# Performance work log

Measured on AMD Instinct MI355X. Metric: run time of the kernel, lower is better.

Reference implementation:

```python
import jax, jax.numpy as jnp
import numpy as np

B, S, D = 4, 2048, 1024   # batch, seq_len, input feature dim
H, E = 16, 64             # head_num, att_embedding_size; H*E = model dim


def setup_inputs() -> dict:
    key = jax.random.key(0)
    ks = jax.random.split(key, 9)
    std = 1.0 / np.sqrt(D)
    M = H * E
    return {
        "x": jax.random.normal(ks[0], (B, S, D), dtype=jnp.float32),
        "Wq": jax.random.normal(ks[1], (D, M), dtype=jnp.float32) * std,
        "bq": jnp.zeros((M,), dtype=jnp.float32),
        "Wk": jax.random.normal(ks[2], (D, M), dtype=jnp.float32) * std,
        "bk": jnp.zeros((M,), dtype=jnp.float32),
        "Wv": jax.random.normal(ks[3], (D, M), dtype=jnp.float32) * std,
        "bv": jnp.zeros((M,), dtype=jnp.float32),
        "Wr": jax.random.normal(ks[4], (D, M), dtype=jnp.float32) * std,
        "br": jnp.zeros((M,), dtype=jnp.float32),
    }


def reference(x, Wq, bq, Wk, bk, Wv, bv, Wr, br):
    # QKV dense layers with ReLU activation (as in the original Keras code)
    qw = jax.nn.relu(x @ Wq + bq)                      # [B,S,H*E]
    kw = jax.nn.relu(x @ Wk + bk)
    vw = jax.nn.relu(x @ Wv + bv)
    # split heads: [B,S,H,E] -> [B,H,S,E]
    qw = qw.reshape(B, S, H, E).transpose(0, 2, 1, 3)
    kw = kw.reshape(B, S, H, E).transpose(0, 2, 1, 3)
    vw = vw.reshape(B, S, H, E).transpose(0, 2, 1, 3)
    # unscaled attention (original has no 1/sqrt(d) scaling)
    a = jnp.einsum("bhqe,bhke->bhqk", qw, kw)          # [B,H,S,S]
    a = jax.nn.softmax(a, axis=-1)
    o = jnp.einsum("bhqk,bhke->bhqe", a, vw)           # [B,H,S,E]
    o = o.transpose(0, 2, 1, 3).reshape(B, S, H * E)
    # residual dense (no activation)
    o = o + (x @ Wr + br)
    return o
```

## Files before the change

kernel.cpp:

```cpp
#include <hip/hip_runtime.h>


typedef __bf16 bf16x8 __attribute__((ext_vector_type(8)));
typedef float  f32x4  __attribute__((ext_vector_type(4)));
typedef short  short8 __attribute__((ext_vector_type(8)));
typedef short  short4v __attribute__((ext_vector_type(4)));
typedef float  float4v __attribute__((ext_vector_type(4)));
typedef int    int4v  __attribute__((ext_vector_type(4)));
typedef unsigned uint2v __attribute__((ext_vector_type(2)));

#define LOG2E 1.44269504088896f

__device__ __forceinline__ unsigned short f2bf(float f) {
  unsigned u = __builtin_bit_cast(unsigned, f);
  u += 0x7fffu + ((u >> 16) & 1u);
  return (unsigned short)(u >> 16);
}

__device__ __forceinline__ unsigned pack2(float lo, float hi) {
  __bf16 a = (__bf16)lo, b = (__bf16)hi;
  unsigned short ua = __builtin_bit_cast(unsigned short, a);
  unsigned short ub = __builtin_bit_cast(unsigned short, b);
  return (unsigned)ua | ((unsigned)ub << 16);
}

__global__ __launch_bounds__(256) void k_cvt_x(const float* __restrict__ x,
                                               short* __restrict__ Xb) {
  const size_t i = ((size_t)blockIdx.x * 256 + threadIdx.x) * 4;
  float4v f = *(const float4v*)(x + i);
  short4v o;
  o[0] = (short)f2bf(f[0]); o[1] = (short)f2bf(f[1]);
  o[2] = (short)f2bf(f[2]); o[3] = (short)f2bf(f[3]);
  *(short4v*)(Xb + i) = o;
}

__global__ __launch_bounds__(256) void k_cvt_w(const float* __restrict__ Wq,
                                               const float* __restrict__ Wk,
                                               const float* __restrict__ Wv,
                                               const float* __restrict__ Wr,
                                               short* __restrict__ Wc) {
  const int bid = blockIdx.x;
  const int w = bid >> 8;
  const int t = bid & 255;
  const int tr = t >> 4, tc = t & 15;
  const float* Ws = (w == 0) ? Wq : (w == 1) ? Wk : (w == 2) ? Wv : Wr;
  __shared__ float T[64][65];
  const int tx = threadIdx.x & 63, ty = threadIdx.x >> 6;
#pragma unroll
  for (int i = 0; i < 16; ++i)
    T[i * 4 + ty][tx] = Ws[(size_t)(tr * 64 + i * 4 + ty) * 1024 + tc * 64 + tx];
  __syncthreads();
#pragma unroll
  for (int i = 0; i < 16; ++i) {
    const int n = tc * 64 + i * 4 + ty;
    Wc[((size_t)w * 1024 + n) * 1024 + tr * 64 + tx] = (short)f2bf(T[tx][i * 4 + ty]);
  }
}

__global__ __launch_bounds__(512, 2) void k_gemm(const short* __restrict__ Xb,
                                                 const short* __restrict__ Wc,
                                                 const float* __restrict__ bq,
                                                 const float* __restrict__ bk2,
                                                 const float* __restrict__ bv,
                                                 const float* __restrict__ br,
                                                 short* __restrict__ Qb,
                                                 short* __restrict__ Kb,
                                                 short* __restrict__ Vt,
                                                 float* __restrict__ Out) {
  __shared__ __align__(16) short smem[65536];
  char* const sb = (char*)smem;
  const int tid = threadIdx.x, wid = tid >> 6, lane = tid & 63;
  const int lr = lane & 15, hi = lane >> 4;
  const int bm = blockIdx.x & 31, bn = blockIdx.x >> 5;
  const int m0 = bm * 256, n0 = bn * 256;
  const int wm = wid >> 2, wn = wid & 3;

  f32x4 acc[8][4] = {};

  const int sl_ = (tid & 7) ^ ((tid >> 3) & 7);
  const int rA0 = ((tid >> 3) << 1) + (sl_ >> 2);
  const short* sa0 = Xb + (size_t)(m0 + rA0) * 1024 + (sl_ & 3) * 8;
  const short* sa1 = Xb + (size_t)(m0 + 128 + rA0) * 1024 + (sl_ & 3) * 8;
  const short* sg0 = Wc + (size_t)(n0 + rA0) * 1024 + (sl_ & 3) * 8;
  const short* sg1 = Wc + (size_t)(n0 + 128 + rA0) * 1024 + (sl_ & 3) * 8;

  const int xr = (((lane & 1) * 4 + hi) ^ ((lr >> 1) & 7)) * 16;
  const int amb = wm * 8192 + (lr >> 1) * 128 + xr;
  const int bnb = 65536 + wn * 4096 + (lr >> 1) * 128 + xr;

#define GLL(SRC, LDSOFF)                                                                   \
  __builtin_amdgcn_global_load_lds((const __attribute__((address_space(1))) void*)(SRC),   \
      (__attribute__((address_space(3))) void*)(sb + (LDSOFF)), 16, 0, 0)

#define STAGE(SLOT)                                                                        \
  do {                                                                                     \
    GLL(sa0, (SLOT) * 16384 + wid * 1024);                                                 \
    GLL(sa1, (SLOT) * 16384 + 8192 + wid * 1024);                                          \
    GLL(sg0, 65536 + (SLOT) * 16384 + wid * 1024);                                         \
    GLL(sg1, 65536 + (SLOT) * 16384 + 8192 + wid * 1024);                                  \
    sa0 += 32; sa1 += 32; sg0 += 32; sg1 += 32;                                            \
  } while (0)

#define PHASE(J, VM, STG)                                                                  \
  do {                                                                                     \
    asm volatile("s_waitcnt vmcnt(" #VM ")" ::: "memory");                                 \
    __builtin_amdgcn_sched_barrier(0);                                                     \
    __builtin_amdgcn_s_barrier();                                                          \
    __builtin_amdgcn_sched_barrier(0);                                                     \
    if (STG) STAGE(((J) + 3) & 3);                                                         \
    bf16x8 am[8], bnr[4];                                                                  \
    _Pragma("unroll")                                                                      \
    for (int mf = 0; mf < 8; ++mf)                                                         \
      am[mf] = *(const bf16x8*)(sb + (((J) & 3) * 16384 + amb + mf * 1024));               \
    _Pragma("unroll")                                                                      \
    for (int nf = 0; nf < 4; ++nf)                                                         \
      bnr[nf] = *(const bf16x8*)(sb + (((J) & 3) * 16384 + bnb + nf * 1024));              \
    asm volatile("s_waitcnt lgkmcnt(0)" ::: "memory");                                     \
    __builtin_amdgcn_sched_barrier(0);                                                     \
    __builtin_amdgcn_s_setprio(1);                                                         \
    _Pragma("unroll")                                                                      \
    for (int mf = 0; mf < 8; ++mf)                                                         \
      _Pragma("unroll")                                                                    \
      for (int nf = 0; nf < 4; ++nf)                                                       \
        acc[mf][nf] = __builtin_amdgcn_mfma_f32_16x16x32_bf16(am[mf], bnr[nf],             \
                                                              acc[mf][nf], 0, 0, 0);      \
    __builtin_amdgcn_s_setprio(0);                                                         \
    __builtin_amdgcn_sched_barrier(0);                                                     \
  } while (0)

  STAGE(0);
  STAGE(1);
  STAGE(2);

  for (int it = 0; it < 7; ++it) {
    PHASE(0, 8, 1);
    PHASE(1, 8, 1);
    PHASE(2, 8, 1);
    PHASE(3, 8, 1);
  }
  PHASE(0, 8, 1);
  PHASE(1, 8, 0);
  PHASE(2, 4, 0);
  PHASE(3, 0, 0);
#undef PHASE
#undef STAGE
#undef GLL

#pragma unroll
  for (int mf = 0; mf < 8; ++mf) {
    const int mbase = m0 + wm * 128 + mf * 16 + hi * 4;
    const int bb2 = mbase >> 11, sbase = mbase & 2047;
#pragma unroll
    for (int nf = 0; nf < 4; ++nf) {
      const int n = n0 + wn * 64 + nf * 16 + lr;
      const float* bp = (n < 2048) ? (n < 1024 ? bq : bk2) : (n < 3072 ? bv : br);
      const float bias = bp[n & 1023];
      float v[4];
#pragma unroll
      for (int r = 0; r < 4; ++r) v[r] = acc[mf][nf][r] + bias;

      if (n < 2048) {
        const int nn = n & 1023, h = nn >> 6, e = nn & 63;
        short* dst = (n < 1024) ? Qb : Kb;
#pragma unroll
        for (int r = 0; r < 4; ++r)
          dst[(((size_t)bb2 * 16 + h) * 2048 + sbase + r) * 64 + e] = (short)f2bf(fmaxf(v[r], 0.f));
      } else if (n < 3072) {
        const int nn = n & 1023, h = nn >> 6, e = nn & 63;
        const int kq = sbase & 31;
        const int Sp = (sbase & ~31) + ((kq >> 2) & 3) * 8 + (kq >> 4) * 4;
        uint2v pv;
        pv[0] = pack2(fmaxf(v[0], 0.f), fmaxf(v[1], 0.f));
        pv[1] = pack2(fmaxf(v[2], 0.f), fmaxf(v[3], 0.f));
        *(uint2v*)&Vt[(((size_t)bb2 * 16 + h) * 64 + e) * 2048 + Sp] = pv;
      } else {
#pragma unroll
        for (int r = 0; r < 4; ++r)
          Out[(size_t)(mbase + r) * 1024 + (n - 3072)] = v[r];
      }
    }
  }
}

__global__ __launch_bounds__(256, 2) void k_attn(const short* __restrict__ Qb,
                                                 const short* __restrict__ Kb,
                                                 const short* __restrict__ Vt,
                                                 float* __restrict__ Out) {
  __shared__ __align__(16) short smem[16384];
  char* const sb = (char*)smem;
  const int tid = threadIdx.x, wid = tid >> 6, lane = tid & 63;
  const int lr = lane & 15, hi = lane >> 4;
  const int bid = ((blockIdx.x & 7) << 6) | (blockIdx.x >> 3);
  const int bh = bid >> 3;
  const int q0 = (bid & 7) * 256;
  const size_t hb = (size_t)bh * (2048 * 64);

  bf16x8 aq[4][2];
#pragma unroll
  for (int g = 0; g < 4; ++g) {
    const short* qp = Qb + hb + (size_t)(q0 + wid * 64 + g * 16 + lr) * 64 + hi * 8;
    aq[g][0] = *(const bf16x8*)qp;
    aq[g][1] = *(const bf16x8*)(qp + 32);
  }

  f32x4 o[4][4] = {};
  float l_run[4] = {0.f, 0.f, 0.f, 0.f};

  const int swz = ((lane & 7) ^ (lane >> 3)) * 8;
  const int rlo = lane >> 3;
  const int wr0 = wid * 16;
  const short* kp0 = Kb + hb + (size_t)(wr0 + rlo) * 64 + swz;
  const short* kp1 = kp0 + 8 * 64;
  const short* vp0 = Vt + hb + (size_t)(wr0 + rlo) * 2048 + swz;
  const short* vp1 = vp0 + 8 * 2048;

  const int vb0 = (lr * 64 + ((hi ^ (lr & 7)) << 3)) * 2;
  const int vb1 = vb0 ^ 64;

#define GLL(SRC, LDSOFF)                                                                   \
  __builtin_amdgcn_global_load_lds((const __attribute__((address_space(1))) void*)(SRC),   \
      (__attribute__((address_space(3))) void*)(sb + (LDSOFF)), 16, 0, 0)

  GLL(kp0, wr0 * 128);
  GLL(kp1, wr0 * 128 + 1024);
  GLL(vp0, 16384 + wr0 * 128);
  GLL(vp1, 16384 + wr0 * 128 + 1024);
  kp0 += 4096; kp1 += 4096; vp0 += 64; vp1 += 64;

  for (int kt = 0; kt < 32; ++kt) {
    const int buf = kt & 1;
    if (kt < 31) {
      const int d = (buf ^ 1) * 8192 + wr0 * 128;
      GLL(kp0, d);
      GLL(kp1, d + 1024);
      GLL(vp0, 16384 + d);
      GLL(vp1, 16384 + d + 1024);
      kp0 += 4096; kp1 += 4096; vp0 += 64; vp1 += 64;
      asm volatile("s_waitcnt vmcnt(4)" ::: "memory");
    } else {
      asm volatile("s_waitcnt vmcnt(0)" ::: "memory");
    }
    __builtin_amdgcn_sched_barrier(0);
    __builtin_amdgcn_s_barrier();
    __builtin_amdgcn_sched_barrier(0);

    f32x4 s[4][4];
    __builtin_amdgcn_s_setprio(1);
#pragma unroll
    for (int kc = 0; kc < 4; ++kc) {
      const bf16x8 kf0 = *(const bf16x8*)(sb + (vb0 + buf * 8192 + kc * 2048));
      const bf16x8 kf1 = *(const bf16x8*)(sb + (vb1 + buf * 8192 + kc * 2048));
#pragma unroll
      for (int g = 0; g < 4; ++g) {
        f32x4 t = __builtin_amdgcn_mfma_f32_16x16x32_bf16(kf0, aq[g][0], (f32x4){0.f, 0.f, 0.f, 0.f}, 0, 0, 0);
        s[g][kc] = __builtin_amdgcn_mfma_f32_16x16x32_bf16(kf1, aq[g][1], t, 0, 0, 0);
      }
    }
    __builtin_amdgcn_s_setprio(0);

    int4v pw[4][2];
#pragma unroll
    for (int g = 0; g < 4; ++g) {
      float sum = 0.f;
#pragma unroll
      for (int kc = 0; kc < 4; ++kc) {
        const float p0 = __builtin_amdgcn_exp2f(s[g][kc][0] * LOG2E);
        const float p1 = __builtin_amdgcn_exp2f(s[g][kc][1] * LOG2E);
        const float p2 = __builtin_amdgcn_exp2f(s[g][kc][2] * LOG2E);
        const float p3 = __builtin_amdgcn_exp2f(s[g][kc][3] * LOG2E);
        sum += (p0 + p1) + (p2 + p3);
        pw[g][kc >> 1][(kc & 1) * 2] = (int)pack2(p0, p1);
        pw[g][kc >> 1][(kc & 1) * 2 + 1] = (int)pack2(p2, p3);
      }
      l_run[g] += sum;
    }

    __builtin_amdgcn_s_setprio(1);
#pragma unroll
    for (int kk = 0; kk < 2; ++kk) {
      const int cb = (kk ? vb1 : vb0) + 16384 + buf * 8192;
#pragma unroll
      for (int et = 0; et < 4; ++et) {
        const bf16x8 vf = *(const bf16x8*)(sb + (cb + et * 2048));
#pragma unroll
        for (int g = 0; g < 4; ++g)
          o[g][et] = __builtin_amdgcn_mfma_f32_16x16x32_bf16(
              vf, __builtin_bit_cast(bf16x8, pw[g][kk]), o[g][et], 0, 0, 0);
      }
    }
    __builtin_amdgcn_s_setprio(0);

    asm volatile("s_waitcnt lgkmcnt(0)" ::: "memory");
    __builtin_amdgcn_sched_barrier(0);
    __builtin_amdgcn_s_barrier();
    __builtin_amdgcn_sched_barrier(0);
  }

  float* Ep = (float*)smem + wid * 1088;
  const int b = bh >> 4, h = bh & 15;
  const int qr = lane >> 2, cc = lane & 3;
#pragma unroll
  for (int g = 0; g < 4; ++g) {
    float lt = l_run[g];
    lt += __shfl_xor(lt, 16);
    lt += __shfl_xor(lt, 32);
    const float inv = 1.0f / lt;
#pragma unroll
    for (int et = 0; et < 4; ++et) {
      f32x4 v = o[g][et] * inv;
      *(float4v*)&Ep[lr * 68 + et * 16 + hi * 4] = v;
    }
    asm volatile("s_waitcnt lgkmcnt(0)" ::: "memory");
    const size_t gb = ((size_t)b * 2048 + q0 + wid * 64 + g * 16 + qr) * 1024 + h * 64 + cc * 4;
#pragma unroll
    for (int i = 0; i < 4; ++i) {
      float4v v = *(const float4v*)&Ep[qr * 68 + cc * 4 + i * 16];
      float4v u = *(const float4v*)&Out[gb + i * 16];
      u += v;
      *(float4v*)&Out[gb + i * 16] = u;
    }
    asm volatile("s_waitcnt lgkmcnt(0)" ::: "memory");
  }
#undef GLL
}

extern "C" void kernel_launch(void* const* d_in, const int* in_sizes, int n_in,
                              void* d_out, int out_size, void* d_ws, size_t ws_size,
                              hipStream_t stream) {
  const float* x  = (const float*)d_in[0];
  const float* Wq = (const float*)d_in[1];
  const float* bq = (const float*)d_in[2];
  const float* Wk = (const float*)d_in[3];
  const float* bk = (const float*)d_in[4];
  const float* Wv = (const float*)d_in[5];
  const float* bv = (const float*)d_in[6];
  const float* Wr = (const float*)d_in[7];
  const float* br = (const float*)d_in[8];
  float* Out = (float*)d_out;

  char* ws = (char*)d_ws;
  short* Xb = (short*)(ws);
  short* Wc = (short*)(ws + (size_t)16 * 1024 * 1024);
  short* Qb = (short*)(ws + (size_t)24 * 1024 * 1024);
  short* Kb = (short*)(ws + (size_t)40 * 1024 * 1024);
  short* Vt = (short*)(ws + (size_t)56 * 1024 * 1024);

  k_cvt_x<<<8192, 256, 0, stream>>>(x, Xb);
  k_cvt_w<<<1024, 256, 0, stream>>>(Wq, Wk, Wv, Wr, Wc);
  k_gemm<<<512, 512, 0, stream>>>(Xb, Wc, bq, bk, bv, br, Qb, Kb, Vt, Out);
  k_attn<<<512, 256, 0, stream>>>(Qb, Kb, Vt, Out);
}
```

Before: 172.8 us.

## Software-pipeline attention: 4-stage LDS ring, overlap QK of next tile with PV

Restructures the attention main loop into a four-slot LDS ring buffer with three tiles in flight. Each iteration issues the QK MFMAs for the next tile together with the PV MFMAs for the current tile, then runs the softmax exp after the barrier, so MFMA work and exp/VALU work can interleave across waves. It also folds LOG2E into Q when Q is written out in the projection kernel, removing a multiply per score. LDS use doubles to 64KB per block, which may reduce occupancy below the two blocks per CU requested by the launch bounds.

```diff
diff --git a/kernel.cpp b/kernel.cpp
--- a/kernel.cpp
+++ b/kernel.cpp
@@ -162,9 +162,11 @@
       if (n < 2048) {
         const int nn = n & 1023, h = nn >> 6, e = nn & 63;
         short* dst = (n < 1024) ? Qb : Kb;
+        const float scale = (n < 1024) ? LOG2E : 1.0f;
 #pragma unroll
         for (int r = 0; r < 4; ++r)
-          dst[(((size_t)bb2 * 16 + h) * 2048 + sbase + r) * 64 + e] = (short)f2bf(fmaxf(v[r], 0.f));
+          dst[(((size_t)bb2 * 16 + h) * 2048 + sbase + r) * 64 + e] =
+              (short)f2bf(fmaxf(v[r], 0.f) * scale);
       } else if (n < 3072) {
         const int nn = n & 1023, h = nn >> 6, e = nn & 63;
         const int kq = sbase & 31;
@@ -186,7 +188,7 @@
                                                  const short* __restrict__ Kb,
                                                  const short* __restrict__ Vt,
                                                  float* __restrict__ Out) {
-  __shared__ __align__(16) short smem[16384];
+  __shared__ __align__(16) short smem[32768];
   char* const sb = (char*)smem;
   const int tid = threadIdx.x, wid = tid >> 6, lane = tid & 63;
   const int lr = lane & 15, hi = lane >> 4;
@@ -205,6 +207,8 @@
 
   f32x4 o[4][4] = {};
   float l_run[4] = {0.f, 0.f, 0.f, 0.f};
+  f32x4 s[4][4];
+  int4v pw[4][2];
 
   const int swz = ((lane & 7) ^ (lane >> 3)) * 8;
   const int rlo = lane >> 3;
@@ -221,80 +225,110 @@
   __builtin_amdgcn_global_load_lds((const __attribute__((address_space(1))) void*)(SRC),   \
       (__attribute__((address_space(3))) void*)(sb + (LDSOFF)), 16, 0, 0)
 
-  GLL(kp0, wr0 * 128);
-  GLL(kp1, wr0 * 128 + 1024);
-  GLL(vp0, 16384 + wr0 * 128);
-  GLL(vp1, 16384 + wr0 * 128 + 1024);
-  kp0 += 4096; kp1 += 4096; vp0 += 64; vp1 += 64;
-
-  for (int kt = 0; kt < 32; ++kt) {
-    const int buf = kt & 1;
-    if (kt < 31) {
-      const int d = (buf ^ 1) * 8192 + wr0 * 128;
-      GLL(kp0, d);
-      GLL(kp1, d + 1024);
-      GLL(vp0, 16384 + d);
-      GLL(vp1, 16384 + d + 1024);
-      kp0 += 4096; kp1 += 4096; vp0 += 64; vp1 += 64;
-      asm volatile("s_waitcnt vmcnt(4)" ::: "memory");
-    } else {
-      asm volatile("s_waitcnt vmcnt(0)" ::: "memory");
-    }
-    __builtin_amdgcn_sched_barrier(0);
-    __builtin_amdgcn_s_barrier();
-    __builtin_amdgcn_sched_barrier(0);
-
-    f32x4 s[4][4];
-    __builtin_amdgcn_s_setprio(1);
-#pragma unroll
-    for (int kc = 0; kc < 4; ++kc) {
-      const bf16x8 kf0 = *(const bf16x8*)(sb + (vb0 + buf * 8192 + kc * 2048));
-      const bf16x8 kf1 = *(const bf16x8*)(sb + (vb1 + buf * 8192 + kc * 2048));
-#pragma unroll
-      for (int g = 0; g < 4; ++g) {
-        f32x4 t = __builtin_amdgcn_mfma_f32_16x16x32_bf16(kf0, aq[g][0], (f32x4){0.f, 0.f, 0.f, 0.f}, 0, 0, 0);
-        s[g][kc] = __builtin_amdgcn_mfma_f32_16x16x32_bf16(kf1, aq[g][1], t, 0, 0, 0);
-      }
-    }
-    __builtin_amdgcn_s_setprio(0);
-
-    int4v pw[4][2];
-#pragma unroll
-    for (int g = 0; g < 4; ++g) {
-      float sum = 0.f;
-#pragma unroll
-      for (int kc = 0; kc < 4; ++kc) {
-        const float p0 = __builtin_amdgcn_exp2f(s[g][kc][0] * LOG2E);
-        const float p1 = __builtin_amdgcn_exp2f(s[g][kc][1] * LOG2E);
-        const float p2 = __builtin_amdgcn_exp2f(s[g][kc][2] * LOG2E);
-        const float p3 = __builtin_amdgcn_exp2f(s[g][kc][3] * LOG2E);
-        sum += (p0 + p1) + (p2 + p3);
-        pw[g][kc >> 1][(kc & 1) * 2] = (int)pack2(p0, p1);
-        pw[g][kc >> 1][(kc & 1) * 2 + 1] = (int)pack2(p2, p3);
-      }
-      l_run[g] += sum;
-    }
-
-    __builtin_amdgcn_s_setprio(1);
-#pragma unroll
-    for (int kk = 0; kk < 2; ++kk) {
-      const int cb = (kk ? vb1 : vb0) + 16384 + buf * 8192;
-#pragma unroll
-      for (int et = 0; et < 4; ++et) {
-        const bf16x8 vf = *(const bf16x8*)(sb + (cb + et * 2048));
-#pragma unroll
-        for (int g = 0; g < 4; ++g)
-          o[g][et] = __builtin_amdgcn_mfma_f32_16x16x32_bf16(
-              vf, __builtin_bit_cast(bf16x8, pw[g][kk]), o[g][et], 0, 0, 0);
-      }
-    }
-    __builtin_amdgcn_s_setprio(0);
-
-    asm volatile("s_waitcnt lgkmcnt(0)" ::: "memory");
-    __builtin_amdgcn_sched_barrier(0);
-    __builtin_amdgcn_s_barrier();
-    __builtin_amdgcn_sched_barrier(0);
-  }
+#define STAGE(SLOT)                                                                        \
+  do {                                                                                     \
+    GLL(kp0, (SLOT) * 8192 + wr0 * 128);                                                   \
+    GLL(kp1, (SLOT) * 8192 + wr0 * 128 + 1024);                                            \
+    GLL(vp0, 32768 + (SLOT) * 8192 + wr0 * 128);                                           \
+    GLL(vp1, 32768 + (SLOT) * 8192 + wr0 * 128 + 1024);                                    \
+    kp0 += 4096; kp1 += 4096; vp0 += 64; vp1 += 64;                                        \
+  } while (0)
+
+#define QK(KS)                                                                             \
+  do {                                                                                     \
+    _Pragma("unroll")                                                                      \
+    for (int kc = 0; kc < 4; ++kc) {                                                       \
+      const bf16x8 kf0 = *(const bf16x8*)(sb + ((KS) * 8192 + vb0 + kc * 2048));           \
+      const bf16x8 kf1 = *(const bf16x8*)(sb + ((KS) * 8192 + vb1 + kc * 2048));           \
+      _Pragma("unroll")                                                                    \
+      for (int g = 0; g < 4; ++g) {                                                        \
+        f32x4 t = __builtin_amdgcn_mfma_f32_16x16x32_bf16(kf0, aq[g][0],                   \
+                                                          (f32x4){0.f, 0.f, 0.f, 0.f},    \
+                                                          0, 0, 0);                        \
+        s[g][kc] = __builtin_amdgcn_mfma_f32_16x16x32_bf16(kf1, aq[g][1], t, 0, 0, 0);     \
+      }                                                                                    \
+    }                                                                                      \
+  } while (0)
+
+#define PV(VS)                                                                             \
+  do {                                                                                     \
+    _Pragma("unroll")                                                                      \
+    for (int kk = 0; kk < 2; ++kk) {                                                       \
+      const int cb = (kk ? vb1 : vb0) + 32768 + (VS) * 8192;                               \
+      _Pragma("unroll")                                                                    \
+      for (int et = 0; et < 4; ++et) {                                                     \
+        const bf16x8 vf = *(const bf16x8*)(sb + (cb + et * 2048));                         \
+        _Pragma("unroll")                                                                  \
+        for (int g = 0; g < 4; ++g)                                                        \
+          o[g][et] = __builtin_amdgcn_mfma_f32_16x16x32_bf16(                              \
+              vf, __builtin_bit_cast(bf16x8, pw[g][kk]), o[g][et], 0, 0, 0);               \
+      }                                                                                    \
+    }                                                                                      \
+  } while (0)
+
+#define SM()                                                                               \
+  do {                                                                                     \
+    _Pragma("unroll")                                                                      \
+    for (int g = 0; g < 4; ++g) {                                                          \
+      float sum = 0.f;                                                                     \
+      _Pragma("unroll")                                                                    \
+      for (int kc = 0; kc < 4; ++kc) {                                                     \
+        const float p0 = __builtin_amdgcn_exp2f(s[g][kc][0]);                              \
+        const float p1 = __builtin_amdgcn_exp2f(s[g][kc][1]);                              \
+        const float p2 = __builtin_amdgcn_exp2f(s[g][kc][2]);                              \
+        const float p3 = __builtin_amdgcn_exp2f(s[g][kc][3]);                              \
+        sum += (p0 + p1) + (p2 + p3);                                                      \
+        pw[g][kc >> 1][(kc & 1) * 2] = (int)pack2(p0, p1);                                 \
+        pw[g][kc >> 1][(kc & 1) * 2 + 1] = (int)pack2(p2, p3);                             \
+      }                                                                                    \
+      l_run[g] += sum;                                                                     \
+    }                                                                                      \
+  } while (0)
+
+#define ITER(J, VM, STG)                                                                   \
+  do {                                                                                     \
+    if (STG) STAGE(((J) + 3) & 3);                                                         \
+    asm volatile("s_waitcnt vmcnt(" #VM ")" ::: "memory");                                 \
+    __builtin_amdgcn_sched_barrier(0);                                                     \
+    __builtin_amdgcn_s_barrier();                                                          \
+    __builtin_amdgcn_sched_barrier(0);                                                     \
+    __builtin_amdgcn_s_setprio(1);                                                         \
+    QK(((J) + 1) & 3);                                                                     \
+    PV((J) & 3);                                                                           \
+    __builtin_amdgcn_s_setprio(0);                                                         \
+    asm volatile("s_waitcnt lgkmcnt(0)" ::: "memory");                                     \
+    __builtin_amdgcn_sched_barrier(0);                                                     \
+    __builtin_amdgcn_s_barrier();                                                          \
+    __builtin_amdgcn_sched_barrier(0);                                                     \
+    SM();                                                                                  \
+  } while (0)
+
+  STAGE(0);
+  STAGE(1);
+  STAGE(2);
+  asm volatile("s_waitcnt vmcnt(8)" ::: "memory");
+  __builtin_amdgcn_sched_barrier(0);
+  __builtin_amdgcn_s_barrier();
+  __builtin_amdgcn_sched_barrier(0);
+  QK(0);
+  SM();
+
+  for (int it = 0; it < 7; ++it) {
+    ITER(0, 8, 1);
+    ITER(1, 8, 1);
+    ITER(2, 8, 1);
+    ITER(3, 8, 1);
+  }
+  ITER(0, 8, 1);
+  ITER(1, 4, 0);
+  ITER(2, 0, 0);
+  PV(3);
+#undef ITER
+#undef SM
+#undef PV
+#undef QK
+#undef STAGE
+#undef GLL
 
   float* Ep = (float*)smem + wid * 1088;
   const int b = bh >> 4, h = bh & 15;
@@ -321,7 +355,6 @@
     }
     asm volatile("s_waitcnt lgkmcnt(0)" ::: "memory");
   }
-#undef GLL
 }
 
 extern "C" void kernel_launch(void* const* d_in, const int* in_sizes, int n_in,
```

Result: slower. 440.8 us (+155.1%).

## Halve attention query tile per block and fold log2e scale into Q

Applied to the files above, without the earlier changes.

The attention kernel now gives each block 128 queries instead of 256, so each warp holds 2 query groups instead of 4. This doubles the grid to 1024 blocks and raises launch bounds to 4 blocks per CU, cutting register pressure to raise occupancy. The log2(e) factor is multiplied into Q in the GEMM epilogue before bf16 rounding, which removes a multiply per score in the softmax loop. In exchange, each K/V tile is loaded from global memory for twice as many blocks, roughly doubling K/V traffic, and pre-scaling Q before rounding changes bf16 precision slightly.

```diff
diff --git a/kernel.cpp b/kernel.cpp
--- a/kernel.cpp
+++ b/kernel.cpp
@@ -162,9 +162,11 @@
       if (n < 2048) {
         const int nn = n & 1023, h = nn >> 6, e = nn & 63;
         short* dst = (n < 1024) ? Qb : Kb;
+        const float scale = (n < 1024) ? LOG2E : 1.0f;
 #pragma unroll
         for (int r = 0; r < 4; ++r)
-          dst[(((size_t)bb2 * 16 + h) * 2048 + sbase + r) * 64 + e] = (short)f2bf(fmaxf(v[r], 0.f));
+          dst[(((size_t)bb2 * 16 + h) * 2048 + sbase + r) * 64 + e] =
+              (short)f2bf(fmaxf(v[r], 0.f) * scale);
       } else if (n < 3072) {
         const int nn = n & 1023, h = nn >> 6, e = nn & 63;
         const int kq = sbase & 31;
@@ -182,7 +184,7 @@
   }
 }
 
-__global__ __launch_bounds__(256, 2) void k_attn(const short* __restrict__ Qb,
+__global__ __launch_bounds__(256, 4) void k_attn(const short* __restrict__ Qb,
                                                  const short* __restrict__ Kb,
                                                  const short* __restrict__ Vt,
                                                  float* __restrict__ Out) {
@@ -190,21 +192,21 @@
   char* const sb = (char*)smem;
   const int tid = threadIdx.x, wid = tid >> 6, lane = tid & 63;
   const int lr = lane & 15, hi = lane >> 4;
-  const int bid = ((blockIdx.x & 7) << 6) | (blockIdx.x >> 3);
-  const int bh = bid >> 3;
-  const int q0 = (bid & 7) * 256;
+  const int bid = ((blockIdx.x & 7) << 7) | (blockIdx.x >> 3);
+  const int bh = bid >> 4;
+  const int q0 = (bid & 15) * 128;
   const size_t hb = (size_t)bh * (2048 * 64);
 
-  bf16x8 aq[4][2];
-#pragma unroll
-  for (int g = 0; g < 4; ++g) {
-    const short* qp = Qb + hb + (size_t)(q0 + wid * 64 + g * 16 + lr) * 64 + hi * 8;
+  bf16x8 aq[2][2];
+#pragma unroll
+  for (int g = 0; g < 2; ++g) {
+    const short* qp = Qb + hb + (size_t)(q0 + wid * 32 + g * 16 + lr) * 64 + hi * 8;
     aq[g][0] = *(const bf16x8*)qp;
     aq[g][1] = *(const bf16x8*)(qp + 32);
   }
 
-  f32x4 o[4][4] = {};
-  float l_run[4] = {0.f, 0.f, 0.f, 0.f};
+  f32x4 o[2][4] = {};
+  float l_run[2] = {0.f, 0.f};
 
   const int swz = ((lane & 7) ^ (lane >> 3)) * 8;
   const int rlo = lane >> 3;
@@ -244,30 +246,29 @@
     __builtin_amdgcn_s_barrier();
     __builtin_amdgcn_sched_barrier(0);
 
-    f32x4 s[4][4];
+    f32x4 s[2][4];
     __builtin_amdgcn_s_setprio(1);
 #pragma unroll
     for (int kc = 0; kc < 4; ++kc) {
       const bf16x8 kf0 = *(const bf16x8*)(sb + (vb0 + buf * 8192 + kc * 2048));
       const bf16x8 kf1 = *(const bf16x8*)(sb + (vb1 + buf * 8192 + kc * 2048));
-#pragma unroll
-      for (int g = 0; g < 4; ++g) {
-        f32x4 t = __builtin_amdgcn_mfma_f32_16x16x32_bf16(kf0, aq[g][0], (f32x4){0.f, 0.f, 0.f, 0.f}, 0, 0, 0);
-        s[g][kc] = __builtin_amdgcn_mfma_f32_16x16x32_bf16(kf1, aq[g][1], t, 0, 0, 0);
-      }
+      f32x4 t0 = __builtin_amdgcn_mfma_f32_16x16x32_bf16(kf0, aq[0][0], (f32x4){0.f, 0.f, 0.f, 0.f}, 0, 0, 0);
+      s[0][kc] = __builtin_amdgcn_mfma_f32_16x16x32_bf16(kf1, aq[0][1], t0, 0, 0, 0);
+      f32x4 t1 = __builtin_amdgcn_mfma_f32_16x16x32_bf16(kf0, aq[1][0], (f32x4){0.f, 0.f, 0.f, 0.f}, 0, 0, 0);
+      s[1][kc] = __builtin_amdgcn_mfma_f32_16x16x32_bf16(kf1, aq[1][1], t1, 0, 0, 0);
     }
     __builtin_amdgcn_s_setprio(0);
 
-    int4v pw[4][2];
-#pragma unroll
-    for (int g = 0; g < 4; ++g) {
+    int4v pw[2][2];
+#pragma unroll
+    for (int g = 0; g < 2; ++g) {
       float sum = 0.f;
 #pragma unroll
       for (int kc = 0; kc < 4; ++kc) {
-        const float p0 = __builtin_amdgcn_exp2f(s[g][kc][0] * LOG2E);
-        const float p1 = __builtin_amdgcn_exp2f(s[g][kc][1] * LOG2E);
-        const float p2 = __builtin_amdgcn_exp2f(s[g][kc][2] * LOG2E);
-        const float p3 = __builtin_amdgcn_exp2f(s[g][kc][3] * LOG2E);
+        const float p0 = __builtin_amdgcn_exp2f(s[g][kc][0]);
+        const float p1 = __builtin_amdgcn_exp2f(s[g][kc][1]);
+        const float p2 = __builtin_amdgcn_exp2f(s[g][kc][2]);
+        const float p3 = __builtin_amdgcn_exp2f(s[g][kc][3]);
         sum += (p0 + p1) + (p2 + p3);
         pw[g][kc >> 1][(kc & 1) * 2] = (int)pack2(p0, p1);
         pw[g][kc >> 1][(kc & 1) * 2 + 1] = (int)pack2(p2, p3);
@@ -278,14 +279,14 @@
     __builtin_amdgcn_s_setprio(1);
 #pragma unroll
     for (int kk = 0; kk < 2; ++kk) {
+      const bf16x8 pa0 = __builtin_bit_cast(bf16x8, pw[0][kk]);
+      const bf16x8 pa1 = __builtin_bit_cast(bf16x8, pw[1][kk]);
       const int cb = (kk ? vb1 : vb0) + 16384 + buf * 8192;
 #pragma unroll
       for (int et = 0; et < 4; ++et) {
         const bf16x8 vf = *(const bf16x8*)(sb + (cb + et * 2048));
-#pragma unroll
-        for (int g = 0; g < 4; ++g)
-          o[g][et] = __builtin_amdgcn_mfma_f32_16x16x32_bf16(
-              vf, __builtin_bit_cast(bf16x8, pw[g][kk]), o[g][et], 0, 0, 0);
+        o[0][et] = __builtin_amdgcn_mfma_f32_16x16x32_bf16(vf, pa0, o[0][et], 0, 0, 0);
+        o[1][et] = __builtin_amdgcn_mfma_f32_16x16x32_bf16(vf, pa1, o[1][et], 0, 0, 0);
       }
     }
     __builtin_amdgcn_s_setprio(0);
@@ -300,7 +301,7 @@
   const int b = bh >> 4, h = bh & 15;
   const int qr = lane >> 2, cc = lane & 3;
 #pragma unroll
-  for (int g = 0; g < 4; ++g) {
+  for (int g = 0; g < 2; ++g) {
     float lt = l_run[g];
     lt += __shfl_xor(lt, 16);
     lt += __shfl_xor(lt, 32);
@@ -311,7 +312,7 @@
       *(float4v*)&Ep[lr * 68 + et * 16 + hi * 4] = v;
     }
     asm volatile("s_waitcnt lgkmcnt(0)" ::: "memory");
-    const size_t gb = ((size_t)b * 2048 + q0 + wid * 64 + g * 16 + qr) * 1024 + h * 64 + cc * 4;
+    const size_t gb = ((size_t)b * 2048 + q0 + wid * 32 + g * 16 + qr) * 1024 + h * 64 + cc * 4;
 #pragma unroll
     for (int i = 0; i < 4; ++i) {
       float4v v = *(const float4v*)&Ep[qr * 68 + cc * 4 + i * 16];
@@ -348,5 +349,5 @@
   k_cvt_x<<<8192, 256, 0, stream>>>(x, Xb);
   k_cvt_w<<<1024, 256, 0, stream>>>(Wq, Wk, Wv, Wr, Wc);
   k_gemm<<<512, 512, 0, stream>>>(Xb, Wc, bq, bk, bv, br, Qb, Kb, Vt, Out);
-  k_attn<<<512, 256, 0, stream>>>(Qb, Kb, Vt, Out);
-}
+  k_attn<<<1024, 256, 0, stream>>>(Qb, Kb, Vt, Out);
+}
```

Result: faster. 166.9 us (-3.4%).
